# Performance work log

Hardware: AMD Instinct MI355X
Metric: run time of the kernel (lower is better)

## Reference

```python
import jax, jax.numpy as jnp
import numpy as np

B, F = 4096, 2048          # batch, inp_dim
H, D = 16, 128             # head_num, head_dim
NB, DB = 16, 8             # BlockLinear: head_dim split into head_num blocks of size head_dim//head_num
KER = 4
PROJ = int((4.0 / 3.0) * H * D)   # 2730
LN_EPS = float(F)          # flax quirk: nn.LayerNorm(inp_dim) sets epsilon positionally -> epsilon = 2048.0
GN_EPS = 1e-6              # flax GroupNorm default epsilon
EPS = 1e-8                 # module eps


def setup_inputs() -> dict:
    key = jax.random.key(0)
    ks = jax.random.split(key, 16)
    s = 0.02  # weight init scale for numerical sanity
    hd = H * D
    d = {}
    d['inputs'] = jax.random.normal(ks[0], (B, F), jnp.float32)
    d['c'] = jax.random.normal(ks[1], (B, hd), jnp.float32)
    d['n'] = jnp.ones((B, hd), jnp.float32)
    d['h'] = jax.random.normal(ks[2], (B, hd), jnp.float32)
    d['m'] = jnp.zeros((B, hd), jnp.float32)
    d['x_prev'] = jax.random.normal(ks[3], (B, KER - 1, F), jnp.float32)
    d['ln_scale'] = jnp.ones((F,), jnp.float32)
    d['ln_bias'] = jnp.zeros((F,), jnp.float32)
    for i, g in enumerate('zifo'):
        d['W' + g + '_k'] = jax.random.normal(ks[4 + i], (F, hd), jnp.float32) * s
        d['W' + g + '_b'] = jnp.zeros((hd,), jnp.float32)
        d['R' + g + '_k'] = jax.random.normal(ks[8 + i], (NB, DB, DB), jnp.float32) * s
        d['R' + g + '_b'] = jnp.zeros((NB, DB), jnp.float32)
    d['gn_scale'] = jnp.ones((D,), jnp.float32)
    d['gn_bias'] = jnp.zeros((D,), jnp.float32)
    d['up_k'] = jax.random.normal(ks[12], (hd, 2 * PROJ), jnp.float32) * s
    d['up_b'] = jnp.zeros((2 * PROJ,), jnp.float32)
    d['down_k'] = jax.random.normal(ks[13], (PROJ, F), jnp.float32) * s
    d['down_b'] = jnp.zeros((F,), jnp.float32)
    return d


def _layer_norm(x, scale, bias, eps):
    mu = x.mean(-1, keepdims=True)
    var = x.var(-1, keepdims=True)
    return (x - mu) / jnp.sqrt(var + eps) * scale + bias


def _group_norm(x, scale, bias, eps):
    # x: (B, H, D); flax GroupNorm(num_groups=H) groups the channel (last) dim,
    # reducing over all non-batch axes within each group.
    b, hh, dd = x.shape
    xg = x.reshape(b, hh, H, dd // H)
    mu = xg.mean(axis=(1, 3), keepdims=True)
    var = xg.var(axis=(1, 3), keepdims=True)
    xn = ((xg - mu) / jnp.sqrt(var + eps)).reshape(b, hh, dd)
    return xn * scale + bias


def reference(inputs, c, n, h, m, x_prev, ln_scale, ln_bias,
              Wz_k, Wz_b, Rz_k, Rz_b, Wi_k, Wi_b, Ri_k, Ri_b,
              Wf_k, Wf_b, Rf_k, Rf_b, Wo_k, Wo_b, Ro_k, Ro_b,
              gn_scale, gn_bias, up_k, up_b, down_k, down_b):
    x_t = _layer_norm(inputs, ln_scale, ln_bias, LN_EPS)
    x_window = jnp.concatenate([x_prev, x_t[:, None, :]], axis=1)  # (B, KER, F)
    x_prev_new = x_window[:, 1:, :]
    x_c = x_t  # use_conv == False

    h4 = h.reshape(B, H, NB, DB)  # per-head block-split hidden

    def gate(Wk, Wb, Rk, Rb):
        rec = jnp.einsum('bhnd,nde->bhne', h4, Rk) + Rb  # block-diagonal recurrence
        return x_c @ Wk + Wb + rec.reshape(B, H * D)

    i_raw = gate(Wi_k, Wi_b, Ri_k, Ri_b)
    f_raw = gate(Wf_k, Wf_b, Rf_k, Rf_b)
    z_raw = gate(Wz_k, Wz_b, Rz_k, Rz_b)
    o_raw = gate(Wo_k, Wo_b, Ro_k, Ro_b)

    logfplusm = m + jax.nn.log_sigmoid(f_raw)
    m_t = jnp.where(jnp.all(n == 0.0, axis=-1, keepdims=True), i_raw,
                    jnp.maximum(i_raw, logfplusm))
    o_t = jax.nn.sigmoid(o_raw)
    i_t = jnp.exp(i_raw - m_t)
    f_t = jnp.exp(logfplusm - m_t)
    z_t = jnp.tanh(z_raw)

    c_t = f_t * c + i_t * z_t
    n_t = f_t * n + i_t
    h_t = o_t * (c_t / (n_t + EPS))

    outn = _group_norm(h_t.reshape(B, H, D), gn_scale, gn_bias, GN_EPS).reshape(B, H * D)
    u = outn @ up_k + up_b
    o1, o2 = jnp.split(u, 2, axis=-1)
    out = (o1 * jax.nn.gelu(o2)) @ down_k + down_b + inputs
    return (out, c_t, n_t, h_t, m_t, x_prev_new)
```

## Files before the change

### kernel.cpp

```cpp
#include <hip/hip_runtime.h>
#include <hip/hip_bf16.h>
#include <cstdint>

#define BB 4096
#define FF 2048
#define HD 2048
#define PROJ_N 2730
#define UPN 5460
#define UPN_PAD 5504
#define DK_PAD 2752

typedef __attribute__((ext_vector_type(8))) short bf16x8;
typedef __attribute__((ext_vector_type(4))) float f32x4;

__device__ __forceinline__ unsigned short f2bf(float f) {
  union { float f; unsigned int u; } x; x.f = f;
  unsigned int r = x.u + 0x7fffu + ((x.u >> 16) & 1u);
  return (unsigned short)(r >> 16);
}

__global__ __launch_bounds__(256) void ln_prep(
    const float* __restrict__ inputs, const float* __restrict__ x_prev,
    const float* __restrict__ n_state,
    const float* __restrict__ ln_scale, const float* __restrict__ ln_bias,
    unsigned short* __restrict__ x_t_bf, float* __restrict__ xprev_out,
    int* __restrict__ flags)
{
  int b = blockIdx.x, t = threadIdx.x;
  const float* row = inputs + ((long)b << 11);
  float x[8];
  {
    float4 a = *(const float4*)(row + t * 8);
    float4 c = *(const float4*)(row + t * 8 + 4);
    x[0]=a.x; x[1]=a.y; x[2]=a.z; x[3]=a.w; x[4]=c.x; x[5]=c.y; x[6]=c.z; x[7]=c.w;
  }
  float s = 0.f, sq = 0.f;
#pragma unroll
  for (int k = 0; k < 8; ++k) { s += x[k]; sq += x[k] * x[k]; }

  const float* nrow = n_state + ((long)b << 11);
  int nz;
  {
    float4 a = *(const float4*)(nrow + t * 8);
    float4 c = *(const float4*)(nrow + t * 8 + 4);
    nz = (a.x != 0.f) | (a.y != 0.f) | (a.z != 0.f) | (a.w != 0.f) |
         (c.x != 0.f) | (c.y != 0.f) | (c.z != 0.f) | (c.w != 0.f);
  }

#pragma unroll
  for (int off = 32; off >= 1; off >>= 1) {
    s  += __shfl_xor(s, off);
    sq += __shfl_xor(sq, off);
  }
  __shared__ float ws_s[4], ws_q[4];
  __shared__ int s_nz;
  if (t == 0) s_nz = 0;
  __syncthreads();
  if (nz) s_nz = 1;
  int wave = t >> 6;
  if ((t & 63) == 0) { ws_s[wave] = s; ws_q[wave] = sq; }
  __syncthreads();
  float ts = ws_s[0] + ws_s[1] + ws_s[2] + ws_s[3];
  float tq = ws_q[0] + ws_q[1] + ws_q[2] + ws_q[3];
  float mu  = ts * (1.f / 2048.f);
  float var = tq * (1.f / 2048.f) - mu * mu;
  float rs  = rsqrtf(var + 2048.0f);

  unsigned short outb[8];
  float y[8];
#pragma unroll
  for (int k = 0; k < 8; ++k) {
    int c = t * 8 + k;
    float v = (x[k] - mu) * rs * ln_scale[c] + ln_bias[c];
    y[k] = v;
    outb[k] = f2bf(v);
  }
  *(uint4*)&x_t_bf[((long)b << 11) + t * 8] = *(uint4*)outb;
  float* xo = xprev_out + (long)b * 6144 + 4096 + t * 8;
  *(float4*)(xo)     = make_float4(y[0], y[1], y[2], y[3]);
  *(float4*)(xo + 4) = make_float4(y[4], y[5], y[6], y[7]);
  const float* src = x_prev + (long)b * 6144 + 2048;
  float* dst = xprev_out + (long)b * 6144;
  for (int i = t; i < 1024; i += 256)
    *(float4*)(dst + i * 4) = *(const float4*)(src + i * 4);
  if (t == 0) flags[b] = (s_nz == 0) ? 1 : 0;
}

__global__ __launch_bounds__(256) void transpose_cast(
    const float* __restrict__ in, unsigned short* __restrict__ out,
    int R, int C, int OC, int OK)
{
  __shared__ float tile[32][33];
  int ro0 = blockIdx.x * 32;
  int co0 = blockIdx.y * 32;
  int tx = threadIdx.x & 31, ty = threadIdx.x >> 5;
#pragma unroll
  for (int i = 0; i < 4; ++i) {
    int r = ro0 + ty + i * 8, cc = co0 + tx;
    float v = (r < R && cc < C) ? in[(long)r * C + cc] : 0.f;
    tile[ty + i * 8][tx] = v;
  }
  __syncthreads();
#pragma unroll
  for (int i = 0; i < 4; ++i) {
    int oc = co0 + ty + i * 8, ok = ro0 + tx;
    if (oc < OC && ok < OK)
      out[(long)oc * OK + ok] = f2bf(tile[tx][ty + i * 8]);
  }
}

#define P_PRE()  do { __builtin_amdgcn_s_barrier(); \
                      asm volatile("s_waitcnt lgkmcnt(0)" ::: "memory"); \
                      __builtin_amdgcn_sched_barrier(0); \
                      __builtin_amdgcn_s_setprio(1); } while (0)
#define P_POST() do { __builtin_amdgcn_s_setprio(0); \
                      __builtin_amdgcn_sched_barrier(0); \
                      __builtin_amdgcn_s_barrier(); \
                      __builtin_amdgcn_sched_barrier(0); } while (0)

#define STAGE_A(h, k2, bo, kt)                                               \
  __builtin_amdgcn_global_load_lds(                                          \
      (const __attribute__((address_space(1))) void*)(pA[h][k2] + (long)(kt)*64), \
      (__attribute__((address_space(3))) void*)(ldsA + (bo) + ((k2)*16384 + (h)*8192) + wvu*1024), \
      16, 0, 0)
#define STAGE_B(cb, i, bo, kt)                                               \
  __builtin_amdgcn_global_load_lds(                                          \
      (const __attribute__((address_space(1))) void*)(pB[cb][i] + (long)(kt)*64), \
      (__attribute__((address_space(3))) void*)(ldsB + (bo) + ((cb)*16384 + (i)*8192) + wvu*1024), \
      16, 0, 0)

#define LOAD_A(rb, bo)                                                       \
  { _Pragma("unroll")                                                        \
    for (int f = 0; f < 4; ++f) {                                            \
      const char* p_ = ldsA + (bo) + (unsigned)((wm*128 + (rb)*64 + f*16 + m16) << 7); \
      aF[f][0] = *(const bf16x8*)(p_ + s0);                                  \
      aF[f][1] = *(const bf16x8*)(p_ + s1);                                  \
    } }
#define LOAD_B(cb, BV, bo)                                                   \
  { _Pragma("unroll")                                                        \
    for (int f = 0; f < 2; ++f) {                                            \
      const char* p_ = ldsB + (bo) + (unsigned)(((cb)*128 + wn*32 + f*16 + m16) << 7); \
      BV[f][0] = *(const bf16x8*)(p_ + s0);                                  \
      BV[f][1] = *(const bf16x8*)(p_ + s1);                                  \
    } }
#define MFMA_PH(rb, cb, BV)                                                  \
  { _Pragma("unroll")                                                        \
    for (int f = 0; f < 4; ++f) {                                            \
      acc[(rb)*4+f][(cb)*2+0] = __builtin_amdgcn_mfma_f32_16x16x32_bf16(     \
          aF[f][0], BV[0][0], acc[(rb)*4+f][(cb)*2+0], 0, 0, 0);             \
      acc[(rb)*4+f][(cb)*2+1] = __builtin_amdgcn_mfma_f32_16x16x32_bf16(     \
          aF[f][0], BV[1][0], acc[(rb)*4+f][(cb)*2+1], 0, 0, 0);             \
      acc[(rb)*4+f][(cb)*2+0] = __builtin_amdgcn_mfma_f32_16x16x32_bf16(     \
          aF[f][1], BV[0][1], acc[(rb)*4+f][(cb)*2+0], 0, 0, 0);             \
      acc[(rb)*4+f][(cb)*2+1] = __builtin_amdgcn_mfma_f32_16x16x32_bf16(     \
          aF[f][1], BV[1][1], acc[(rb)*4+f][(cb)*2+1], 0, 0, 0);             \
    } }

__global__ __launch_bounds__(512) void gemm8(
    const unsigned short* __restrict__ A, const unsigned short* __restrict__ Bt,
    float* __restrict__ C, int K, int lda, int ldb, int ldc,
    int Nreal, int NBmax,
    const float* __restrict__ bias, const float* __restrict__ resid,
    long strideB, long strideC)
{
  __shared__ __attribute__((aligned(1024))) char smem[131072];
  char* ldsA = smem;
  char* ldsB = smem + 65536;

  Bt += (long)blockIdx.z * strideB;
  C  += (long)blockIdx.z * strideC;

  const int tid  = threadIdx.x;
  const int lane = tid & 63, wvu = tid >> 6;
  const int wm = wvu >> 2, wn = wvu & 3;
  const int m16 = lane & 15, qd = lane >> 4;

  int nwg = gridDim.x * gridDim.y;
  int lin = blockIdx.y * gridDim.x + blockIdx.x;
  int qq_ = nwg >> 3, rr_ = nwg & 7, xcd = lin & 7, idx8 = lin >> 3;
  int swz = (xcd < rr_ ? xcd * (qq_ + 1) : rr_ * (qq_ + 1) + (xcd - rr_) * qq_) + idx8;
  int bx = swz % gridDim.x, by = swz / gridDim.x;
  const int n0 = bx * 256, m0 = by * 256;

  const int l8 = lane >> 3, l7 = lane & 7;
  const int scol = ((l7 ^ l8) << 3);
  const unsigned short *pA[2][2], *pB[2][2];
#pragma unroll
  for (int h = 0; h < 2; ++h)
#pragma unroll
    for (int k2 = 0; k2 < 2; ++k2) {
      int row = m0 + k2 * 128 + h * 64 + wvu * 8 + l8;
      pA[h][k2] = A + (long)row * lda + scol;
    }
#pragma unroll
  for (int cb = 0; cb < 2; ++cb)
#pragma unroll
    for (int i = 0; i < 2; ++i) {
      int qq = i * 64 + wvu * 8 + l8;
      int n  = ((qq >> 5) << 6) + cb * 32 + (qq & 31);
      int gr = n0 + n; if (gr > NBmax - 1) gr = NBmax - 1;
      pB[cb][i] = Bt + (long)gr * ldb + scol;
    }

  const int s0 = ((qd ^ (m16 & 7)) << 4);
  const int s1 = s0 ^ 64;

  f32x4 acc[8][4] = {};
  bf16x8 aF[4][2], b0v[2][2], b1v[2][2];

  const int NT = K >> 6;
  const int tp = (NT > 1) ? 1 : 0;

  STAGE_A(0,0,0,0); STAGE_A(0,1,0,0);
  STAGE_B(0,0,0,0); STAGE_B(0,1,0,0);
  STAGE_B(1,0,0,0); STAGE_B(1,1,0,0);
  STAGE_A(1,0,0,0); STAGE_A(1,1,0,0);
  STAGE_A(0,0,32768,tp); STAGE_A(0,1,32768,tp);
  STAGE_B(0,0,32768,tp); STAGE_B(0,1,32768,tp);
  STAGE_B(1,0,32768,tp); STAGE_B(1,1,32768,tp);
  STAGE_A(1,0,32768,tp); STAGE_A(1,1,32768,tp);
  asm volatile("s_waitcnt vmcnt(8)" ::: "memory");
  __builtin_amdgcn_s_barrier();
  __builtin_amdgcn_sched_barrier(0);

  for (int t = 0; t < NT; ++t) {
    const int co = (t & 1) << 15;
    const int t2 = (t + 2 < NT) ? t + 2 : NT - 1;
    LOAD_A(0, co);
    LOAD_B(0, b0v, co);
    P_PRE(); MFMA_PH(0,0,b0v); P_POST();
    LOAD_B(1, b1v, co);
    STAGE_A(0,0,co,t2); STAGE_A(0,1,co,t2);
    P_PRE(); MFMA_PH(0,1,b1v); P_POST();
    LOAD_A(1, co);
    STAGE_B(0,0,co,t2); STAGE_B(0,1,co,t2);
    STAGE_B(1,0,co,t2); STAGE_B(1,1,co,t2);
    P_PRE(); MFMA_PH(1,1,b1v); P_POST();
    STAGE_A(1,0,co,t2); STAGE_A(1,1,co,t2);
    asm volatile("s_waitcnt vmcnt(8)" ::: "memory");
    P_PRE(); MFMA_PH(1,0,b0v); P_POST();
  }
  asm volatile("s_waitcnt vmcnt(0)" ::: "memory");

#pragma unroll
  for (int mf = 0; mf < 8; ++mf) {
    int gm = m0 + wm * 128 + mf * 16 + qd * 4;
#pragma unroll
    for (int nf = 0; nf < 4; ++nf) {
      int gn = n0 + wn * 64 + nf * 16 + m16;
      if (gn < Nreal) {
        float badd = bias ? bias[gn] : 0.f;
#pragma unroll
        for (int r = 0; r < 4; ++r) {
          float v = acc[mf][nf][r] + badd;
          if (resid) v += resid[(long)(gm + r) * ldc + gn];
          C[(long)(gm + r) * ldc + gn] = v;
        }
      }
    }
  }
}

__global__ __launch_bounds__(256) void slstm_pointwise(
    const float* __restrict__ g_i, const float* __restrict__ g_f,
    const float* __restrict__ g_z, const float* __restrict__ g_o,
    const float* __restrict__ Wib, const float* __restrict__ Wfb,
    const float* __restrict__ Wzb, const float* __restrict__ Wob,
    const float* __restrict__ Ri, const float* __restrict__ Rf,
    const float* __restrict__ Rz, const float* __restrict__ Ro,
    const float* __restrict__ Rib, const float* __restrict__ Rfb,
    const float* __restrict__ Rzb, const float* __restrict__ Rob,
    const float* __restrict__ c_in, const float* __restrict__ n_in,
    const float* __restrict__ h_in, const float* __restrict__ m_in,
    const int* __restrict__ flags,
    float* __restrict__ c_out, float* __restrict__ n_out,
    float* __restrict__ h_out, float* __restrict__ m_out)
{
  int idx = blockIdx.x * 256 + threadIdx.x;
  int b = idx >> 11, j = idx & 2047;
  int hh = j >> 7, nb = (j >> 3) & 15, e = j & 7;
  const float* hp = h_in + ((long)b << 11) + hh * 128 + nb * 8;
  float hv[8];
#pragma unroll
  for (int d = 0; d < 8; ++d) hv[d] = hp[d];
  int rb = nb * 64 + e;
  float reci = Rib[nb * 8 + e], recf = Rfb[nb * 8 + e];
  float recz = Rzb[nb * 8 + e], reco = Rob[nb * 8 + e];
#pragma unroll
  for (int d = 0; d < 8; ++d) {
    reci += hv[d] * Ri[rb + d * 8];
    recf += hv[d] * Rf[rb + d * 8];
    recz += hv[d] * Rz[rb + d * 8];
    reco += hv[d] * Ro[rb + d * 8];
  }
  float iraw = g_i[idx] + Wib[j] + reci;
  float fraw = g_f[idx] + Wfb[j] + recf;
  float zraw = g_z[idx] + Wzb[j] + recz;
  float oraw = g_o[idx] + Wob[j] + reco;
  float mo = m_in[idx];
  float ls = fminf(fraw, 0.f) - log1pf(expf(-fabsf(fraw)));
  float lfpm = mo + ls;
  float mt = flags[b] ? iraw : fmaxf(iraw, lfpm);
  float ot = 1.f / (1.f + expf(-oraw));
  float it = expf(iraw - mt);
  float ft = expf(lfpm - mt);
  float zt = tanhf(zraw);
  float ct = ft * c_in[idx] + it * zt;
  float nt = ft * n_in[idx] + it;
  float ht = ot * ct / (nt + 1e-8f);
  c_out[idx] = ct; n_out[idx] = nt; h_out[idx] = ht; m_out[idx] = mt;
}

__global__ __launch_bounds__(256) void groupnorm(
    const float* __restrict__ h_t, const float* __restrict__ gn_scale,
    const float* __restrict__ gn_bias, unsigned short* __restrict__ outn)
{
  int b = blockIdx.x, t = threadIdx.x;
  const float* row = h_t + ((long)b << 11);
  float x[8];
  {
    float4 a = *(const float4*)(row + t * 8);
    float4 c = *(const float4*)(row + t * 8 + 4);
    x[0]=a.x; x[1]=a.y; x[2]=a.z; x[3]=a.w; x[4]=c.x; x[5]=c.y; x[6]=c.z; x[7]=c.w;
  }
  float s = 0.f, sq = 0.f;
#pragma unroll
  for (int k = 0; k < 8; ++k) { s += x[k]; sq += x[k] * x[k]; }
  __shared__ float s1[256], s2[256];
  s1[t] = s; s2[t] = sq;
  __syncthreads();
  for (int st = 128; st >= 16; st >>= 1) {
    if (t < st) { s1[t] += s1[t + st]; s2[t] += s2[t + st]; }
    __syncthreads();
  }
  int g = t & 15;
  float mu  = s1[g] * (1.f / 128.f);
  float var = s2[g] * (1.f / 128.f) - mu * mu;
  float rs  = rsqrtf(var + 1e-6f);
  unsigned short ob[8];
#pragma unroll
  for (int k = 0; k < 8; ++k) {
    int j = t * 8 + k;
    int dd = j & 127;
    ob[k] = f2bf((x[k] - mu) * rs * gn_scale[dd] + gn_bias[dd]);
  }
  *(uint4*)&outn[((long)b << 11) + t * 8] = *(uint4*)ob;
}

__global__ __launch_bounds__(256) void gelu_mult(
    const float* __restrict__ u, const float* __restrict__ up_b,
    unsigned short* __restrict__ Hg)
{
  int idx = blockIdx.x * 256 + threadIdx.x;
  if (idx >= BB * DK_PAD) return;
  int b = idx / DK_PAD, p = idx - b * DK_PAD;
  unsigned short r = 0;
  if (p < PROJ_N) {
    const float* ur = u + (long)b * UPN_PAD;
    float o1 = ur[p] + up_b[p];
    float o2 = ur[PROJ_N + p] + up_b[PROJ_N + p];
    float tt = o2 + 0.044715f * o2 * o2 * o2;
    float g = 0.5f * o2 * (1.f + tanhf(0.7978845608028654f * tt));
    r = f2bf(o1 * g);
  }
  Hg[idx] = r;
}

extern "C" void kernel_launch(void* const* d_in, const int* in_sizes, int n_in,
                              void* d_out, int out_size, void* d_ws, size_t ws_size,
                              hipStream_t stream)
{
  const float* inputs  = (const float*)d_in[0];
  const float* c_in    = (const float*)d_in[1];
  const float* n_st    = (const float*)d_in[2];
  const float* h_in    = (const float*)d_in[3];
  const float* m_in    = (const float*)d_in[4];
  const float* x_prev  = (const float*)d_in[5];
  const float* ln_s    = (const float*)d_in[6];
  const float* ln_b    = (const float*)d_in[7];
  const float* Wz = (const float*)d_in[8];  const float* Wzb = (const float*)d_in[9];
  const float* Rz = (const float*)d_in[10]; const float* Rzb = (const float*)d_in[11];
  const float* Wi = (const float*)d_in[12]; const float* Wib = (const float*)d_in[13];
  const float* Ri = (const float*)d_in[14]; const float* Rib = (const float*)d_in[15];
  const float* Wf = (const float*)d_in[16]; const float* Wfb = (const float*)d_in[17];
  const float* Rf = (const float*)d_in[18]; const float* Rfb = (const float*)d_in[19];
  const float* Wo = (const float*)d_in[20]; const float* Wob = (const float*)d_in[21];
  const float* Ro = (const float*)d_in[22]; const float* Rob = (const float*)d_in[23];
  const float* gn_s = (const float*)d_in[24]; const float* gn_b = (const float*)d_in[25];
  const float* up_k = (const float*)d_in[26]; const float* up_b = (const float*)d_in[27];
  const float* dn_k = (const float*)d_in[28]; const float* dn_b = (const float*)d_in[29];

  char* ws = (char*)d_ws;
  float* g_raw = (float*)ws;
  float* u_buf = (float*)ws;
  unsigned short* x_t_bf = (unsigned short*)(ws + 134217728);
  unsigned short* outn_bf = x_t_bf;
  unsigned short* Wt  = (unsigned short*)(ws + 150994944);
  unsigned short* upT = (unsigned short*)(ws + 184549376);
  unsigned short* Hg  = upT;
  unsigned short* dkT = (unsigned short*)(ws + 207093760);
  int* flags = (int*)(ws + 218365952);

  float* out   = (float*)d_out;
  float* out_c = out + (long)1 * 8388608;
  float* out_n = out + (long)2 * 8388608;
  float* out_h = out + (long)3 * 8388608;
  float* out_m = out + (long)4 * 8388608;
  float* out_xp = out + (long)5 * 8388608;

  ln_prep<<<BB, 256, 0, stream>>>(inputs, x_prev, n_st, ln_s, ln_b, x_t_bf, out_xp, flags);

  transpose_cast<<<dim3(64, 64), 256, 0, stream>>>(Wi, Wt + 0L * 4194304, 2048, 2048, 2048, 2048);
  transpose_cast<<<dim3(64, 64), 256, 0, stream>>>(Wf, Wt + 1L * 4194304, 2048, 2048, 2048, 2048);
  transpose_cast<<<dim3(64, 64), 256, 0, stream>>>(Wz, Wt + 2L * 4194304, 2048, 2048, 2048, 2048);
  transpose_cast<<<dim3(64, 64), 256, 0, stream>>>(Wo, Wt + 3L * 4194304, 2048, 2048, 2048, 2048);
  transpose_cast<<<dim3(64, 172), 256, 0, stream>>>(up_k, upT, 2048, UPN, UPN_PAD, 2048);
  transpose_cast<<<dim3(86, 64), 256, 0, stream>>>(dn_k, dkT, PROJ_N, 2048, 2048, DK_PAD);

  gemm8<<<dim3(8, 16, 4), 512, 0, stream>>>(x_t_bf, Wt, g_raw,
      2048, 2048, 2048, 2048, 2048, 2048, nullptr, nullptr, 4194304L, 8388608L);

  slstm_pointwise<<<32768, 256, 0, stream>>>(
      g_raw, g_raw + 8388608L, g_raw + 2L * 8388608, g_raw + 3L * 8388608,
      Wib, Wfb, Wzb, Wob, Ri, Rf, Rz, Ro, Rib, Rfb, Rzb, Rob,
      c_in, n_st, h_in, m_in, flags, out_c, out_n, out_h, out_m);

  groupnorm<<<BB, 256, 0, stream>>>(out_h, gn_s, gn_b, outn_bf);

  gemm8<<<dim3(22, 16, 1), 512, 0, stream>>>(outn_bf, upT, u_buf,
      2048, 2048, 2048, UPN_PAD, UPN_PAD, UPN_PAD, nullptr, nullptr, 0L, 0L);

  gelu_mult<<<(BB * DK_PAD) / 256, 256, 0, stream>>>(u_buf, up_b, Hg);

  gemm8<<<dim3(8, 16, 1), 512, 0, stream>>>(Hg, dkT, out,
      DK_PAD, DK_PAD, DK_PAD, 2048, 2048, 2048, dn_b, inputs, 0L, 0L);
}
```

Before: 1.118 ms.

## Fuse GELU gating into up-projection GEMM epilogue and merge pointwise with groupnorm

The up-projection weights are now transposed into interleaved 16-column pairs, so each GEMM tile holds matching o1 and o2 columns. The GEMM epilogue can then apply the bias, the tanh-GELU and the product, and write bf16 H directly. This removes the fp32 write and re-read of the large up-projection output and one launch. Separately, the sLSTM pointwise and groupnorm kernels are merged into one per-row kernel using vectorized loads, which avoids re-reading h from memory. In exchange, the padding grows (PROJ_PAD 2816), so the down GEMM does slightly more K work and the up GEMM slightly more N work.

```diff
diff --git a/kernel.cpp b/kernel.cpp
--- a/kernel.cpp
+++ b/kernel.cpp
@@ -7,8 +7,8 @@
 #define HD 2048
 #define PROJ_N 2730
 #define UPN 5460
-#define UPN_PAD 5504
-#define DK_PAD 2752
+#define PROJ_PAD 2816
+#define UPN_PAIR 5632
 
 typedef __attribute__((ext_vector_type(8))) short bf16x8;
 typedef __attribute__((ext_vector_type(4))) float f32x4;
@@ -106,6 +106,32 @@
     int oc = co0 + ty + i * 8, ok = ro0 + tx;
     if (oc < OC && ok < OK)
       out[(long)oc * OK + ok] = f2bf(tile[tx][ty + i * 8]);
+  }
+}
+
+__global__ __launch_bounds__(256) void transpose_cast_pair(
+    const float* __restrict__ in, unsigned short* __restrict__ out)
+{
+  __shared__ float tile[32][33];
+  int ro0 = blockIdx.x * 32;
+  int co0 = blockIdx.y * 32;
+  int tx = threadIdx.x & 31, ty = threadIdx.x >> 5;
+#pragma unroll
+  for (int i = 0; i < 4; ++i) {
+    int r = ro0 + ty + i * 8, cc = co0 + tx;
+    float v = (cc < UPN) ? in[(long)r * UPN + cc] : 0.f;
+    tile[ty + i * 8][tx] = v;
+  }
+  __syncthreads();
+#pragma unroll
+  for (int i = 0; i < 4; ++i) {
+    int oc = co0 + ty + i * 8, ok = ro0 + tx;
+    if (oc < UPN) {
+      int pos = (oc < PROJ_N)
+        ? ((oc >> 4) * 32 + (oc & 15))
+        : (((oc - PROJ_N) >> 4) * 32 + 16 + ((oc - PROJ_N) & 15));
+      out[(long)pos * 2048 + ok] = f2bf(tile[tx][ty + i * 8]);
+    }
   }
 }
 
@@ -161,7 +187,8 @@
     float* __restrict__ C, int K, int lda, int ldb, int ldc,
     int Nreal, int NBmax,
     const float* __restrict__ bias, const float* __restrict__ resid,
-    long strideB, long strideC)
+    long strideB, long strideC,
+    int gmode, unsigned short* __restrict__ Hp, const float* __restrict__ upb)
 {
   __shared__ __attribute__((aligned(1024))) char smem[131072];
   char* ldsA = smem;
@@ -242,26 +269,50 @@
   }
   asm volatile("s_waitcnt vmcnt(0)" ::: "memory");
 
-#pragma unroll
-  for (int mf = 0; mf < 8; ++mf) {
-    int gm = m0 + wm * 128 + mf * 16 + qd * 4;
-#pragma unroll
-    for (int nf = 0; nf < 4; ++nf) {
-      int gn = n0 + wn * 64 + nf * 16 + m16;
-      if (gn < Nreal) {
-        float badd = bias ? bias[gn] : 0.f;
-#pragma unroll
-        for (int r = 0; r < 4; ++r) {
-          float v = acc[mf][nf][r] + badd;
-          if (resid) v += resid[(long)(gm + r) * ldc + gn];
-          C[(long)(gm + r) * ldc + gn] = v;
+  if (gmode == 0) {
+#pragma unroll
+    for (int mf = 0; mf < 8; ++mf) {
+      int gm = m0 + wm * 128 + mf * 16 + qd * 4;
+#pragma unroll
+      for (int nf = 0; nf < 4; ++nf) {
+        int gn = n0 + wn * 64 + nf * 16 + m16;
+        if (gn < Nreal) {
+          float badd = bias ? bias[gn] : 0.f;
+#pragma unroll
+          for (int r = 0; r < 4; ++r) {
+            float v = acc[mf][nf][r] + badd;
+            if (resid) v += resid[(long)(gm + r) * ldc + gn];
+            C[(long)(gm + r) * ldc + gn] = v;
+          }
         }
       }
     }
-  }
-}
-
-__global__ __launch_bounds__(256) void slstm_pointwise(
+  } else {
+    const int pbase = ((n0 + wn * 64) >> 5) * 16 + m16;
+#pragma unroll
+    for (int pp = 0; pp < 2; ++pp) {
+      int p = pbase + pp * 16;
+      bool valid = p < PROJ_N;
+      float b1 = valid ? upb[p] : 0.f;
+      float b2 = valid ? upb[PROJ_N + p] : 0.f;
+#pragma unroll
+      for (int mf = 0; mf < 8; ++mf) {
+        int gm = m0 + wm * 128 + mf * 16 + qd * 4;
+#pragma unroll
+        for (int r = 0; r < 4; ++r) {
+          float o1 = acc[mf][2*pp][r] + b1;
+          float o2 = acc[mf][2*pp+1][r] + b2;
+          float tt = o2 + 0.044715f * o2 * o2 * o2;
+          float g = 0.5f * o2 * (1.f + tanhf(0.7978845608028654f * tt));
+          unsigned short hw = valid ? f2bf(o1 * g) : (unsigned short)0;
+          Hp[(long)(gm + r) * PROJ_PAD + p] = hw;
+        }
+      }
+    }
+  }
+}
+
+__global__ __launch_bounds__(256) void slstm_gn(
     const float* __restrict__ g_i, const float* __restrict__ g_f,
     const float* __restrict__ g_z, const float* __restrict__ g_o,
     const float* __restrict__ Wib, const float* __restrict__ Wfb,
@@ -273,59 +324,65 @@
     const float* __restrict__ c_in, const float* __restrict__ n_in,
     const float* __restrict__ h_in, const float* __restrict__ m_in,
     const int* __restrict__ flags,
+    const float* __restrict__ gn_scale, const float* __restrict__ gn_bias,
     float* __restrict__ c_out, float* __restrict__ n_out,
-    float* __restrict__ h_out, float* __restrict__ m_out)
-{
-  int idx = blockIdx.x * 256 + threadIdx.x;
-  int b = idx >> 11, j = idx & 2047;
-  int hh = j >> 7, nb = (j >> 3) & 15, e = j & 7;
+    float* __restrict__ h_out, float* __restrict__ m_out,
+    unsigned short* __restrict__ outn)
+{
+  int b = blockIdx.x, t = threadIdx.x;
+  long base = ((long)b << 11) + t * 8;
+  int nb = t & 15, hh = t >> 4;
   const float* hp = h_in + ((long)b << 11) + hh * 128 + nb * 8;
   float hv[8];
-#pragma unroll
-  for (int d = 0; d < 8; ++d) hv[d] = hp[d];
-  int rb = nb * 64 + e;
-  float reci = Rib[nb * 8 + e], recf = Rfb[nb * 8 + e];
-  float recz = Rzb[nb * 8 + e], reco = Rob[nb * 8 + e];
-#pragma unroll
-  for (int d = 0; d < 8; ++d) {
-    reci += hv[d] * Ri[rb + d * 8];
-    recf += hv[d] * Rf[rb + d * 8];
-    recz += hv[d] * Rz[rb + d * 8];
-    reco += hv[d] * Ro[rb + d * 8];
-  }
-  float iraw = g_i[idx] + Wib[j] + reci;
-  float fraw = g_f[idx] + Wfb[j] + recf;
-  float zraw = g_z[idx] + Wzb[j] + recz;
-  float oraw = g_o[idx] + Wob[j] + reco;
-  float mo = m_in[idx];
-  float ls = fminf(fraw, 0.f) - log1pf(expf(-fabsf(fraw)));
-  float lfpm = mo + ls;
-  float mt = flags[b] ? iraw : fmaxf(iraw, lfpm);
-  float ot = 1.f / (1.f + expf(-oraw));
-  float it = expf(iraw - mt);
-  float ft = expf(lfpm - mt);
-  float zt = tanhf(zraw);
-  float ct = ft * c_in[idx] + it * zt;
-  float nt = ft * n_in[idx] + it;
-  float ht = ot * ct / (nt + 1e-8f);
-  c_out[idx] = ct; n_out[idx] = nt; h_out[idx] = ht; m_out[idx] = mt;
-}
-
-__global__ __launch_bounds__(256) void groupnorm(
-    const float* __restrict__ h_t, const float* __restrict__ gn_scale,
-    const float* __restrict__ gn_bias, unsigned short* __restrict__ outn)
-{
-  int b = blockIdx.x, t = threadIdx.x;
-  const float* row = h_t + ((long)b << 11);
-  float x[8];
   {
-    float4 a = *(const float4*)(row + t * 8);
-    float4 c = *(const float4*)(row + t * 8 + 4);
-    x[0]=a.x; x[1]=a.y; x[2]=a.z; x[3]=a.w; x[4]=c.x; x[5]=c.y; x[6]=c.z; x[7]=c.w;
-  }
+    float4 a = *(const float4*)hp, c2 = *(const float4*)(hp + 4);
+    hv[0]=a.x; hv[1]=a.y; hv[2]=a.z; hv[3]=a.w; hv[4]=c2.x; hv[5]=c2.y; hv[6]=c2.z; hv[7]=c2.w;
+  }
+  int fl = flags[b];
+  int rb0 = nb * 64;
+  float recI[8], recF[8], recZ[8], recO[8];
+#pragma unroll
+  for (int e = 0; e < 8; ++e) {
+    float ri = Rib[nb*8+e], rf = Rfb[nb*8+e], rz = Rzb[nb*8+e], ro = Rob[nb*8+e];
+#pragma unroll
+    for (int d = 0; d < 8; ++d) {
+      float h = hv[d];
+      ri += h * Ri[rb0 + d*8 + e];
+      rf += h * Rf[rb0 + d*8 + e];
+      rz += h * Rz[rb0 + d*8 + e];
+      ro += h * Ro[rb0 + d*8 + e];
+    }
+    recI[e] = ri; recF[e] = rf; recZ[e] = rz; recO[e] = ro;
+  }
+  float gi[8], gf[8], gz[8], go[8], ci[8], ni[8], mi[8];
+#define LD8(dst, src) { float4 a_ = *(const float4*)((src)); float4 b_ = *(const float4*)((src) + 4); \
+    dst[0]=a_.x; dst[1]=a_.y; dst[2]=a_.z; dst[3]=a_.w; dst[4]=b_.x; dst[5]=b_.y; dst[6]=b_.z; dst[7]=b_.w; }
+  LD8(gi, g_i + base); LD8(gf, g_f + base); LD8(gz, g_z + base); LD8(go, g_o + base);
+  LD8(ci, c_in + base); LD8(ni, n_in + base); LD8(mi, m_in + base);
+  float wi[8], wf[8], wz[8], wo[8];
+  LD8(wi, Wib + t*8); LD8(wf, Wfb + t*8); LD8(wz, Wzb + t*8); LD8(wo, Wob + t*8);
+#undef LD8
+  float ht[8], co_[8], no_[8], mo_[8];
   float s = 0.f, sq = 0.f;
 #pragma unroll
-  for (int k = 0; k < 8; ++k) { s += x[k]; sq += x[k] * x[k]; }
+  for (int e = 0; e < 8; ++e) {
+    float iraw = gi[e] + wi[e] + recI[e];
+    float fraw = gf[e] + wf[e] + recF[e];
+    float zraw = gz[e] + wz[e] + recZ[e];
+    float oraw = go[e] + wo[e] + recO[e];
+    float ls = fminf(fraw, 0.f) - log1pf(expf(-fabsf(fraw)));
+    float lfpm = mi[e] + ls;
+    float mt = fl ? iraw : fmaxf(iraw, lfpm);
+    float ot = 1.f / (1.f + expf(-oraw));
+    float it = expf(iraw - mt);
+    float ft = expf(lfpm - mt);
+    float zt = tanhf(zraw);
+    float ct = ft * ci[e] + it * zt;
+    float nt = ft * ni[e] + it;
+    float h = ot * ct / (nt + 1e-8f);
+    ht[e] = h; co_[e] = ct; no_[e] = nt; mo_[e] = mt;
+    s += h; sq += h * h;
+  }
   __shared__ float s1[256], s2[256];
   s1[t] = s; s2[t] = sq;
   __syncthreads();
@@ -333,37 +390,21 @@
     if (t < st) { s1[t] += s1[t + st]; s2[t] += s2[t + st]; }
     __syncthreads();
   }
-  int g = t & 15;
-  float mu  = s1[g] * (1.f / 128.f);
-  float var = s2[g] * (1.f / 128.f) - mu * mu;
+  float mu  = s1[nb] * (1.f / 128.f);
+  float var = s2[nb] * (1.f / 128.f) - mu * mu;
   float rs  = rsqrtf(var + 1e-6f);
+#define ST8(dst, src) { *(float4*)(dst) = make_float4(src[0],src[1],src[2],src[3]); \
+    *(float4*)((dst)+4) = make_float4(src[4],src[5],src[6],src[7]); }
+  ST8(c_out + base, co_); ST8(n_out + base, no_);
+  ST8(h_out + base, ht);  ST8(m_out + base, mo_);
+#undef ST8
   unsigned short ob[8];
 #pragma unroll
-  for (int k = 0; k < 8; ++k) {
-    int j = t * 8 + k;
-    int dd = j & 127;
-    ob[k] = f2bf((x[k] - mu) * rs * gn_scale[dd] + gn_bias[dd]);
-  }
-  *(uint4*)&outn[((long)b << 11) + t * 8] = *(uint4*)ob;
-}
-
-__global__ __launch_bounds__(256) void gelu_mult(
-    const float* __restrict__ u, const float* __restrict__ up_b,
-    unsigned short* __restrict__ Hg)
-{
-  int idx = blockIdx.x * 256 + threadIdx.x;
-  if (idx >= BB * DK_PAD) return;
-  int b = idx / DK_PAD, p = idx - b * DK_PAD;
-  unsigned short r = 0;
-  if (p < PROJ_N) {
-    const float* ur = u + (long)b * UPN_PAD;
-    float o1 = ur[p] + up_b[p];
-    float o2 = ur[PROJ_N + p] + up_b[PROJ_N + p];
-    float tt = o2 + 0.044715f * o2 * o2 * o2;
-    float g = 0.5f * o2 * (1.f + tanhf(0.7978845608028654f * tt));
-    r = f2bf(o1 * g);
-  }
-  Hg[idx] = r;
+  for (int e = 0; e < 8; ++e) {
+    int dd = (t * 8 + e) & 127;
+    ob[e] = f2bf((ht[e] - mu) * rs * gn_scale[dd] + gn_bias[dd]);
+  }
+  *(uint4*)&outn[base] = *(uint4*)ob;
 }
 
 extern "C" void kernel_launch(void* const* d_in, const int* in_sizes, int n_in,
@@ -392,14 +433,13 @@
 
   char* ws = (char*)d_ws;
   float* g_raw = (float*)ws;
-  float* u_buf = (float*)ws;
   unsigned short* x_t_bf = (unsigned short*)(ws + 134217728);
   unsigned short* outn_bf = x_t_bf;
   unsigned short* Wt  = (unsigned short*)(ws + 150994944);
   unsigned short* upT = (unsigned short*)(ws + 184549376);
-  unsigned short* Hg  = upT;
-  unsigned short* dkT = (unsigned short*)(ws + 207093760);
-  int* flags = (int*)(ws + 218365952);
+  unsigned short* Hg  = (unsigned short*)(ws + 207618048);
+  unsigned short* dkT = (unsigned short*)(ws + 230686720);
+  int* flags = (int*)(ws + 242221056);
 
   float* out   = (float*)d_out;
   float* out_c = out + (long)1 * 8388608;
@@ -414,24 +454,24 @@
   transpose_cast<<<dim3(64, 64), 256, 0, stream>>>(Wf, Wt + 1L * 4194304, 2048, 2048, 2048, 2048);
   transpose_cast<<<dim3(64, 64), 256, 0, stream>>>(Wz, Wt + 2L * 4194304, 2048, 2048, 2048, 2048);
   transpose_cast<<<dim3(64, 64), 256, 0, stream>>>(Wo, Wt + 3L * 4194304, 2048, 2048, 2048, 2048);
-  transpose_cast<<<dim3(64, 172), 256, 0, stream>>>(up_k, upT, 2048, UPN, UPN_PAD, 2048);
-  transpose_cast<<<dim3(86, 64), 256, 0, stream>>>(dn_k, dkT, PROJ_N, 2048, 2048, DK_PAD);
+  transpose_cast_pair<<<dim3(64, 171), 256, 0, stream>>>(up_k, upT);
+  transpose_cast<<<dim3(88, 64), 256, 0, stream>>>(dn_k, dkT, PROJ_N, 2048, 2048, PROJ_PAD);
 
   gemm8<<<dim3(8, 16, 4), 512, 0, stream>>>(x_t_bf, Wt, g_raw,
-      2048, 2048, 2048, 2048, 2048, 2048, nullptr, nullptr, 4194304L, 8388608L);
-
-  slstm_pointwise<<<32768, 256, 0, stream>>>(
+      2048, 2048, 2048, 2048, 2048, 2048, nullptr, nullptr, 4194304L, 8388608L,
+      0, nullptr, nullptr);
+
+  slstm_gn<<<BB, 256, 0, stream>>>(
       g_raw, g_raw + 8388608L, g_raw + 2L * 8388608, g_raw + 3L * 8388608,
       Wib, Wfb, Wzb, Wob, Ri, Rf, Rz, Ro, Rib, Rfb, Rzb, Rob,
-      c_in, n_st, h_in, m_in, flags, out_c, out_n, out_h, out_m);
-
-  groupnorm<<<BB, 256, 0, stream>>>(out_h, gn_s, gn_b, outn_bf);
-
-  gemm8<<<dim3(22, 16, 1), 512, 0, stream>>>(outn_bf, upT, u_buf,
-      2048, 2048, 2048, UPN_PAD, UPN_PAD, UPN_PAD, nullptr, nullptr, 0L, 0L);
-
-  gelu_mult<<<(BB * DK_PAD) / 256, 256, 0, stream>>>(u_buf, up_b, Hg);
+      c_in, n_st, h_in, m_in, flags, gn_s, gn_b,
+      out_c, out_n, out_h, out_m, outn_bf);
+
+  gemm8<<<dim3(UPN_PAIR / 256, 16, 1), 512, 0, stream>>>(outn_bf, upT, nullptr,
+      2048, 2048, 2048, 0, UPN_PAIR, UPN_PAIR, nullptr, nullptr, 0L, 0L,
+      1, Hg, up_b);
 
   gemm8<<<dim3(8, 16, 1), 512, 0, stream>>>(Hg, dkT, out,
-      DK_PAD, DK_PAD, DK_PAD, 2048, 2048, 2048, dn_b, inputs, 0L, 0L);
-}
+      PROJ_PAD, PROJ_PAD, PROJ_PAD, 2048, 2048, 2048, dn_b, inputs, 0L, 0L,
+      0, nullptr, nullptr);
+}
```

Result: slower. 1.189 ms (+6.3%).
